# Optimization experiments

Measured on AMD Instinct MI355X. Metric: run time of the kernel, lower is better.

The kernel has to match this reference:

```python
import jax, jax.numpy as jnp
import numpy as np


def _squash(s, axis=-1, eps=1e-8):
    # squash(s) = |s|^2/(1+|s|^2) * s/|s|
    s2 = jnp.sum(s * s, axis=axis, keepdims=True)
    return (s2 / (1.0 + s2)) * s / jnp.sqrt(s2 + eps)


def _conv(x, w, b, stride):
    y = jax.lax.conv_general_dilated(
        x, w, (stride, stride), 'VALID',
        dimension_numbers=('NCHW', 'OIHW', 'NCHW'))
    return y + b[None, :, None, None]


def setup_inputs() -> dict:
    key = jax.random.key(0)
    ks = jax.random.split(key, 4)
    B = 64
    sc = 0.05
    return {
        'x': jax.random.normal(ks[0], (B, 3, 32, 32), jnp.float32),
        'conv_w': jax.random.normal(ks[1], (256, 3, 9, 9), jnp.float32) * sc,
        'conv_b': jnp.zeros((256,), jnp.float32),
        'pcap_w': jax.random.normal(ks[2], (256, 256, 9, 9), jnp.float32) * sc,
        'pcap_b': jnp.zeros((256,), jnp.float32),
        'W': jax.random.normal(ks[3], (100, 2048, 16, 8), jnp.float32) * sc,
    }


def reference(x, conv_w, conv_b, pcap_w, pcap_b, W):
    # Conv stem: [B,3,32,32] -> [B,256,24,24]
    h = jax.nn.relu(_conv(x, conv_w, conv_b, 1))
    # PrimaryCaps conv: [B,256,24,24] -> [B,256,8,8], then view to capsules
    p = _conv(h, pcap_w, pcap_b, 2)
    u = _squash(p.reshape(p.shape[0], 2048, 8))            # [B,2048,8]
    # DenseCapsule: u_hat[b,o,i,d] = W[o,i,d,k] u[b,i,k]
    u_hat = jnp.einsum('oidk,bik->boid', W, u)             # [B,100,2048,16]
    u_hat_sg = jax.lax.stop_gradient(u_hat)
    b = jnp.zeros(u_hat.shape[:3], u_hat.dtype)            # [B,100,2048]
    routings = 3
    v = None
    for i in range(routings):
        c = jax.nn.softmax(b, axis=1)                      # over out caps
        uh = u_hat if i == routings - 1 else u_hat_sg
        v = _squash(jnp.einsum('boi,boid->bod', c, uh))    # [B,100,16]
        if i < routings - 1:
            b = b + jnp.einsum('bod,boid->boi', v, u_hat_sg)
    return v
```

## Files before the change

### kernel.cpp

```cpp
#include <hip/hip_runtime.h>

#define NB 64
#define NO 100
#define NI 2048
#define ND 16
#define NK 8

#define WS_H    0
#define WS_U    9437184
#define WS_BB   10485760
#define WS_CB   23592960
#define WS_SP   36700160
#define WS_V    38338560
#define WS_PP   WS_BB

typedef __attribute__((ext_vector_type(8))) short bf16x8;
typedef __attribute__((ext_vector_type(16))) float f32x16;
typedef __attribute__((ext_vector_type(4))) float f32x4;

__device__ inline unsigned short f2bf(float x) {
    union { float f; unsigned u; } v; v.f = x;
    unsigned r = (v.u + 0x7FFFu + ((v.u >> 16) & 1u)) >> 16;
    return (unsigned short)r;
}
__device__ inline float bf2f(unsigned short h) {
    union { unsigned u; float f; } v; v.u = ((unsigned)h) << 16;
    return v.f;
}

__global__ __launch_bounds__(256) void conv1_kernel(const float* __restrict__ x,
        const float* __restrict__ w, const float* __restrict__ bias,
        unsigned short* __restrict__ h_hi, unsigned short* __restrict__ h_lo) {
    const int b = blockIdx.x;
    const int ocg = blockIdx.y;
    __shared__ float xl[3 * 32 * 32];
    __shared__ float wl[16 * 243];
    const int tid = threadIdx.x;
    for (int idx = tid; idx < 3072; idx += 256) xl[idx] = x[b * 3072 + idx];
    for (int idx = tid; idx < 16 * 243; idx += 256)
        wl[idx] = w[ocg * 16 * 243 + idx];
    __syncthreads();
    const int lane = tid & 63;
    const int wg = tid >> 6;
    float acc[4][9];
    #pragma unroll
    for (int jj = 0; jj < 4; ++jj) {
        float bv = bias[ocg * 16 + wg * 4 + jj];
        #pragma unroll
        for (int j = 0; j < 9; ++j) acc[jj][j] = bv;
    }
    int xbase[9];
    #pragma unroll
    for (int j = 0; j < 9; ++j) {
        int p = lane + 64 * j;
        xbase[j] = (p / 24) * 32 + (p % 24);
    }
    for (int ic = 0; ic < 3; ++ic)
        for (int ky = 0; ky < 9; ++ky) {
            #pragma unroll
            for (int kx = 0; kx < 9; ++kx) {
                float wv[4];
                #pragma unroll
                for (int jj = 0; jj < 4; ++jj)
                    wv[jj] = wl[(wg * 4 + jj) * 243 + ic * 81 + ky * 9 + kx];
                #pragma unroll
                for (int j = 0; j < 9; ++j) {
                    float xv = xl[ic * 1024 + xbase[j] + ky * 32 + kx];
                    #pragma unroll
                    for (int jj = 0; jj < 4; ++jj)
                        acc[jj][j] = fmaf(xv, wv[jj], acc[jj][j]);
                }
            }
        }
    #pragma unroll
    for (int jj = 0; jj < 4; ++jj) {
        int oc = ocg * 16 + wg * 4 + jj;
        #pragma unroll
        for (int j = 0; j < 9; ++j) {
            int p = lane + 64 * j;
            float v = fmaxf(acc[jj][j], 0.f);
            unsigned short hi = f2bf(v);
            unsigned short lo = f2bf(v - bf2f(hi));
            size_t o = (size_t)(b * 256 + oc) * 576 + p;
            h_hi[o] = hi;
            h_lo[o] = lo;
        }
    }
}

__global__ __launch_bounds__(256) void wb_precompute_kernel(const float* __restrict__ w,
        unsigned short* __restrict__ wBhi, unsigned short* __restrict__ wBlo) {
    const int ic = blockIdx.x;
    const int ocq = blockIdx.y;
    __shared__ float tl[64][85];
    const int tid = threadIdx.x;
    for (int f = tid; f < 5184; f += 256) {
        int oc = f / 81, kk = f % 81;
        tl[oc][kk] = w[(size_t)(ocq * 64 + oc) * 20736 + ic * 81 + kk];
    }
    __syncthreads();
    for (int idx = tid; idx < 9216; idx += 256) {
        int ky = idx >> 10;
        int rem = idx & 1023;
        int ocl = rem >> 4;
        int kx = rem & 15;
        float val = (kx < 9) ? tl[ocl][ky * 9 + kx] : 0.f;
        unsigned short hi = f2bf(val);
        unsigned short lo = f2bf(val - bf2f(hi));
        size_t dst = ((size_t)(ic * 9 + ky) * 256 + ocq * 64 + ocl) * 16 + kx;
        wBhi[dst] = hi;
        wBlo[dst] = lo;
    }
}

__global__ __launch_bounds__(256) void conv2_mfma_kernel(
        const unsigned short* __restrict__ h_hi, const unsigned short* __restrict__ h_lo,
        const unsigned short* __restrict__ wBhi, const unsigned short* __restrict__ wBlo,
        float* __restrict__ pp) {
    const int bpair = blockIdx.x;
    const int ocb = blockIdx.y;
    const int ks = blockIdx.z;
    __shared__ __align__(16) unsigned short Ahi[128 * 20];
    __shared__ __align__(16) unsigned short Alo[128 * 20];
    __shared__ __align__(16) unsigned short Bhi[128 * 20];
    __shared__ __align__(16) unsigned short Blo[128 * 20];
    const int tid = threadIdx.x;
    const int lane = tid & 63;
    const int wid = tid >> 6;
    const int wr = wid >> 1, wc = wid & 1;
    const int l31 = lane & 31, kh = lane >> 5;
    const int slot = tid & 127;
    const int role = tid >> 7;
    const int oy = (slot >> 3) & 7;
    const int ox = slot & 7;
    const unsigned short* hsel = role ? h_lo : h_hi;
    const size_t hrow0 = ((size_t)(bpair * 2 + (slot >> 6)) * 256) * 576;

    f32x16 acc[2][2];
    #pragma unroll
    for (int m = 0; m < 2; ++m)
        #pragma unroll
        for (int n = 0; n < 2; ++n)
            #pragma unroll
            for (int r = 0; r < 16; ++r) acc[m][n][r] = 0.f;

#define LDS64(arr, off, dst) { union { struct { uint2 a, b; } p; bf16x8 v; } u_;           \
    u_.p.a = *(const uint2*)((arr) + (off));                                               \
    u_.p.b = *(const uint2*)((arr) + (off) + 4);                                           \
    dst = u_.v; }

    const int ic0 = ks * 32;
    for (int ic = ic0; ic < ic0 + 32; ++ic) {
        const size_t wb_ic = (size_t)ic * 36864;
        const size_t h_ic = hrow0 + (size_t)ic * 576;
        #pragma unroll 1
        for (int ky = 0; ky < 9; ++ky) {
            __syncthreads();
            {
                const uint4* Ash = (const uint4*)(wBhi + wb_ic + (size_t)ky * 4096 + ocb * 2048);
                const uint4* Asl = (const uint4*)(wBlo + wb_ic + (size_t)ky * 4096 + ocb * 2048);
                uint4 va = Ash[tid];
                uint4 vb = Asl[tid];
                const int row = tid >> 1, half = tid & 1;
                unsigned short* dh = Ahi + row * 20 + half * 8;
                unsigned short* dl = Alo + row * 20 + half * 8;
                uint2 a0; a0.x = va.x; a0.y = va.y;
                uint2 a1; a1.x = va.z; a1.y = va.w;
                uint2 b0; b0.x = vb.x; b0.y = vb.y;
                uint2 b1; b1.x = vb.z; b1.y = vb.w;
                *(uint2*)dh = a0; *(uint2*)(dh + 4) = a1;
                *(uint2*)dl = b0; *(uint2*)(dl + 4) = b1;
            }
            {
                const unsigned int* hp =
                    (const unsigned int*)(hsel + h_ic + (2 * oy + ky) * 24 + 2 * ox);
                unsigned int d0 = hp[0], d1 = hp[1], d2 = hp[2], d3 = hp[3], d4 = hp[4];
                unsigned short* Bdst = (role ? Blo : Bhi) + slot * 20;
                uint2 p0; p0.x = d0; p0.y = d1;
                uint2 p1; p1.x = d2; p1.y = d3;
                uint2 p2; p2.x = d4 & 0xFFFFu; p2.y = 0u;
                uint2 p3; p3.x = 0u; p3.y = 0u;
                *(uint2*)Bdst = p0; *(uint2*)(Bdst + 4) = p1;
                *(uint2*)(Bdst + 8) = p2; *(uint2*)(Bdst + 12) = p3;
            }
            __syncthreads();
            bf16x8 ah[2], al[2], bh[2], bl[2];
            #pragma unroll
            for (int m = 0; m < 2; ++m) {
                const int rowoff = (wr * 64 + m * 32 + l31) * 20 + kh * 8;
                LDS64(Ahi, rowoff, ah[m]);
                LDS64(Alo, rowoff, al[m]);
            }
            #pragma unroll
            for (int n = 0; n < 2; ++n) {
                const int coloff = (wc * 64 + n * 32 + l31) * 20 + kh * 8;
                LDS64(Bhi, coloff, bh[n]);
                LDS64(Blo, coloff, bl[n]);
            }
            #pragma unroll
            for (int m = 0; m < 2; ++m)
                #pragma unroll
                for (int n = 0; n < 2; ++n) {
                    acc[m][n] = __builtin_amdgcn_mfma_f32_32x32x16_bf16(
                        ah[m], bh[n], acc[m][n], 0, 0, 0);
                    acc[m][n] = __builtin_amdgcn_mfma_f32_32x32x16_bf16(
                        ah[m], bl[n], acc[m][n], 0, 0, 0);
                    acc[m][n] = __builtin_amdgcn_mfma_f32_32x32x16_bf16(
                        al[m], bh[n], acc[m][n], 0, 0, 0);
                }
        }
    }
#undef LDS64
    #pragma unroll
    for (int m = 0; m < 2; ++m)
        #pragma unroll
        for (int n = 0; n < 2; ++n) {
            const int slotg = wc * 64 + n * 32 + l31;
            const int b = bpair * 2 + (slotg >> 6);
            const int pos = slotg & 63;
            #pragma unroll
            for (int r = 0; r < 16; ++r) {
                const int row = (r & 3) + 8 * (r >> 2) + 4 * kh;
                const int oc = ocb * 128 + wr * 64 + m * 32 + row;
                pp[(((size_t)ks * 64 + b) * 256 + oc) * 64 + pos] = acc[m][n][r];
            }
        }
}

__global__ __launch_bounds__(256) void reduce_bias_squash_kernel(
        const float* __restrict__ pp, const float* __restrict__ bias,
        float* __restrict__ u) {
    const int cap = blockIdx.x * 256 + threadIdx.x;
    const int b = cap >> 11;
    const int rem = cap & 2047;
    const int oc = rem >> 3;
    const int oy = rem & 7;
    float4 sa = {0.f, 0.f, 0.f, 0.f}, sb = {0.f, 0.f, 0.f, 0.f};
    #pragma unroll
    for (int ks = 0; ks < 8; ++ks) {
        const float4* p4 = (const float4*)&pp[(((size_t)ks * 64 + b) * 256 + oc) * 64 + oy * 8];
        float4 a = p4[0], c = p4[1];
        sa.x += a.x; sa.y += a.y; sa.z += a.z; sa.w += a.w;
        sb.x += c.x; sb.y += c.y; sb.z += c.z; sb.w += c.w;
    }
    const float bv = bias[oc];
    sa.x += bv; sa.y += bv; sa.z += bv; sa.w += bv;
    sb.x += bv; sb.y += bv; sb.z += bv; sb.w += bv;
    float s2 = sa.x * sa.x + sa.y * sa.y + sa.z * sa.z + sa.w * sa.w
             + sb.x * sb.x + sb.y * sb.y + sb.z * sb.z + sb.w * sb.w;
    float scale = (s2 / (1.f + s2)) / sqrtf(s2 + 1e-8f);
    sa.x *= scale; sa.y *= scale; sa.z *= scale; sa.w *= scale;
    sb.x *= scale; sb.y *= scale; sb.z *= scale; sb.w *= scale;
    float4* up = (float4*)&u[(size_t)cap * 8];
    up[0] = sa;
    up[1] = sb;
}

__global__ __launch_bounds__(256) void transpose_u_kernel(const float* __restrict__ u,
        float* __restrict__ ut) {
    const int blk = blockIdx.x;
    __shared__ float tl[64 * 132];
    const int tid = threadIdx.x;
    #pragma unroll
    for (int rep = 0; rep < 8; ++rep) {
        const int idx = tid + 256 * rep;
        const int b = idx >> 5, q = idx & 31;
        float4 uv = *(const float4*)(u + (size_t)b * 16384 + blk * 128 + 4 * q);
        *(float4*)&tl[b * 132 + 4 * q] = uv;
    }
    __syncthreads();
    #pragma unroll
    for (int rep = 0; rep < 32; ++rep) {
        const int row = rep * 4 + (tid >> 6);
        const int b = tid & 63;
        ut[(size_t)(blk * 128 + row) * 64 + b] = tl[b * 132 + row];
    }
}

template <int UNIFORM>
__global__ __launch_bounds__(256) void r_weighted_mfma_kernel(
        const float* __restrict__ W, const float* __restrict__ u,
        const float* __restrict__ cbuf, float* __restrict__ sp) {
    const int o = blockIdx.x;
    const int st = blockIdx.y;
    __shared__ __align__(16) unsigned short Ahi[16 * 72];
    __shared__ __align__(16) unsigned short Alo[16 * 72];
    __shared__ __align__(16) unsigned short Bhi[64 * 72];
    __shared__ __align__(16) unsigned short Blo[64 * 72];
    const int tid = threadIdx.x;
    const int lane = tid & 63;
    const int w = tid >> 6;
    const int l15 = lane & 15;
    const int hi = lane >> 4;
    const int sb = tid >> 2;
    const int si = tid & 3;
    f32x4 acc = {0.f, 0.f, 0.f, 0.f};
    const float* Wo = W + (size_t)o * 262144;
    const int i_base = st * 256;
    #pragma unroll 1
    for (int iter = 0; iter < 32; ++iter) {
        const int i0 = i_base + iter * 8;
        __syncthreads();
        {
            float4 wv = *(const float4*)(Wo + (size_t)i0 * 128 + 4 * tid);
            const int i_l = tid >> 5;
            const int d = (tid >> 1) & 15;
            const int k0 = (tid & 1) * 4;
            unsigned short* dh = Ahi + d * 72 + i_l * 8 + k0;
            unsigned short* dl = Alo + d * 72 + i_l * 8 + k0;
            float vv[4] = {wv.x, wv.y, wv.z, wv.w};
            unsigned int h01, h23, l01, l23;
            unsigned short h, l;
            h = f2bf(vv[0]); l = f2bf(vv[0] - bf2f(h)); h01 = h; l01 = l;
            h = f2bf(vv[1]); l = f2bf(vv[1] - bf2f(h)); h01 |= (unsigned)h << 16; l01 |= (unsigned)l << 16;
            h = f2bf(vv[2]); l = f2bf(vv[2] - bf2f(h)); h23 = h; l23 = l;
            h = f2bf(vv[3]); l = f2bf(vv[3] - bf2f(h)); h23 |= (unsigned)h << 16; l23 |= (unsigned)l << 16;
            *(unsigned int*)dh = h01; *(unsigned int*)(dh + 2) = h23;
            *(unsigned int*)dl = l01; *(unsigned int*)(dl + 2) = l23;
        }
        #pragma unroll
        for (int half = 0; half < 2; ++half) {
            const int i_l = si + 4 * half;
            const float* up = u + (size_t)sb * 16384 + (size_t)(i0 + i_l) * 8;
            float4 u0 = *(const float4*)up;
            float4 u1 = *(const float4*)(up + 4);
            float cv = UNIFORM ? 0.01f
                               : cbuf[(size_t)sb * (NO * NI) + o * NI + i0 + i_l];
            float q[8] = {u0.x * cv, u0.y * cv, u0.z * cv, u0.w * cv,
                          u1.x * cv, u1.y * cv, u1.z * cv, u1.w * cv};
            uint4 ph, pl;
            unsigned short h0, h1, l0, l1;
            h0 = f2bf(q[0]); l0 = f2bf(q[0] - bf2f(h0));
            h1 = f2bf(q[1]); l1 = f2bf(q[1] - bf2f(h1));
            ph.x = h0 | ((unsigned)h1 << 16); pl.x = l0 | ((unsigned)l1 << 16);
            h0 = f2bf(q[2]); l0 = f2bf(q[2] - bf2f(h0));
            h1 = f2bf(q[3]); l1 = f2bf(q[3] - bf2f(h1));
            ph.y = h0 | ((unsigned)h1 << 16); pl.y = l0 | ((unsigned)l1 << 16);
            h0 = f2bf(q[4]); l0 = f2bf(q[4] - bf2f(h0));
            h1 = f2bf(q[5]); l1 = f2bf(q[5] - bf2f(h1));
            ph.z = h0 | ((unsigned)h1 << 16); pl.z = l0 | ((unsigned)l1 << 16);
            h0 = f2bf(q[6]); l0 = f2bf(q[6] - bf2f(h0));
            h1 = f2bf(q[7]); l1 = f2bf(q[7] - bf2f(h1));
            ph.w = h0 | ((unsigned)h1 << 16); pl.w = l0 | ((unsigned)l1 << 16);
            *(uint4*)(Bhi + sb * 72 + i_l * 8) = ph;
            *(uint4*)(Blo + sb * 72 + i_l * 8) = pl;
        }
        __syncthreads();
        #pragma unroll
        for (int ch = 0; ch < 2; ++ch) {
            bf16x8 ah = *(const bf16x8*)(Ahi + l15 * 72 + ch * 32 + hi * 8);
            bf16x8 al = *(const bf16x8*)(Alo + l15 * 72 + ch * 32 + hi * 8);
            bf16x8 bh = *(const bf16x8*)(Bhi + (w * 16 + l15) * 72 + ch * 32 + hi * 8);
            bf16x8 bl = *(const bf16x8*)(Blo + (w * 16 + l15) * 72 + ch * 32 + hi * 8);
            acc = __builtin_amdgcn_mfma_f32_16x16x32_bf16(ah, bh, acc, 0, 0, 0);
            acc = __builtin_amdgcn_mfma_f32_16x16x32_bf16(ah, bl, acc, 0, 0, 0);
            acc = __builtin_amdgcn_mfma_f32_16x16x32_bf16(al, bh, acc, 0, 0, 0);
        }
    }
    const int bg = w * 16 + l15;
    float4 st4;
    st4.x = acc[0]; st4.y = acc[1]; st4.z = acc[2]; st4.w = acc[3];
    *(float4*)&sp[(((size_t)o * 8 + st) * 64 + bg) * 16 + hi * 4] = st4;
}

__global__ __launch_bounds__(256) void squash_v_kernel(const float* __restrict__ sp,
        float* __restrict__ dest) {
    const int t = blockIdx.x * 256 + threadIdx.x;
    const int d = t & 15;
    const int cap = t >> 4;
    const int o = cap >> 6;
    const int bb = cap & 63;
    float s = 0.f;
    #pragma unroll
    for (int st = 0; st < 8; ++st)
        s += sp[(((size_t)o * 8 + st) * 64 + bb) * 16 + d];
    float s2 = s * s;
    #pragma unroll
    for (int off = 1; off < 16; off <<= 1)
        s2 += __shfl_xor(s2, off, 16);
    float scale = (s2 / (1.f + s2)) / sqrtf(s2 + 1e-8f);
    dest[(bb * NO + o) * ND + d] = s * scale;
}

template <int ADD>
__global__ __launch_bounds__(256) void r_logits_mfma_kernel(
        const float* __restrict__ W, const float* __restrict__ ut,
        const float* __restrict__ v, float* __restrict__ bbuf) {
    const int o = blockIdx.x;
    const int st = blockIdx.y;
    __shared__ __align__(16) unsigned short Aext[128 * 40];
    __shared__ __align__(16) unsigned short B1[64 * 40];
    __shared__ __align__(16) unsigned short B2[64 * 40];
    __shared__ float ul[128 * 66];
    const int tid = threadIdx.x;
    const int lane = tid & 63;
    const int w = tid >> 6;
    const int l15 = lane & 15;
    const int hi = lane >> 4;
    const float* Wo = W + (size_t)o * 262144;
    {
        const int b = tid >> 2;
        const int dq = (tid & 3) * 4;
        float4 vv = *(const float4*)&v[((size_t)b * NO + o) * ND + dq];
        float q[4] = {vv.x, vv.y, vv.z, vv.w};
        #pragma unroll
        for (int c = 0; c < 4; ++c) {
            unsigned short h = f2bf(q[c]);
            unsigned short l = f2bf(q[c] - bf2f(h));
            B1[b * 40 + dq + c] = h;
            B1[b * 40 + 16 + dq + c] = h;
            B2[b * 40 + dq + c] = l;
            B2[b * 40 + 16 + dq + c] = 0;
        }
    }
    __syncthreads();
    #pragma unroll 1
    for (int iter = 0; iter < 8; ++iter) {
        __syncthreads();
        #pragma unroll
        for (int rep = 0; rep < 2; ++rep) {
            const int slot = rep * 256 + tid;
            const int i_l = slot >> 5;
            const int dgrp = (slot >> 3) & 3;
            const int k = slot & 7;
            const float* src = Wo + (size_t)(st * 128 + iter * 16 + i_l) * 128
                             + dgrp * 32 + k;
            float v0 = src[0], v1 = src[8], v2 = src[16], v3 = src[24];
            unsigned short h0 = f2bf(v0), l0 = f2bf(v0 - bf2f(h0));
            unsigned short h1 = f2bf(v1), l1 = f2bf(v1 - bf2f(h1));
            unsigned short h2 = f2bf(v2), l2 = f2bf(v2 - bf2f(h2));
            unsigned short h3 = f2bf(v3), l3 = f2bf(v3 - bf2f(h3));
            uint2 ph; ph.x = h0 | ((unsigned)h1 << 16); ph.y = h2 | ((unsigned)h3 << 16);
            uint2 pl; pl.x = l0 | ((unsigned)l1 << 16); pl.y = l2 | ((unsigned)l3 << 16);
            unsigned short* dst = Aext + (i_l * 8 + k) * 40 + dgrp * 4;
            *(uint2*)dst = ph;
            *(uint2*)(dst + 16) = pl;
        }
        const int base_row = (st * 128 + iter * 16) * 8;
        #pragma unroll
        for (int rep = 0; rep < 8; ++rep) {
            const int idx = tid + 256 * rep;
            const int row = idx >> 4, bq = idx & 15;
            float4 uv = *(const float4*)(ut + (size_t)(base_row + row) * 64 + 4 * bq);
            *(float4*)&ul[row * 66 + 4 * bq] = uv;
        }
        __syncthreads();
        f32x4 acc[8];
        bf16x8 bf1 = *(const bf16x8*)&B1[(w * 16 + l15) * 40 + hi * 8];
        bf16x8 bf2 = *(const bf16x8*)&B2[(w * 16 + l15) * 40 + hi * 8];
        #pragma unroll
        for (int mt = 0; mt < 8; ++mt) {
            f32x4 z = {0.f, 0.f, 0.f, 0.f};
            bf16x8 af = *(const bf16x8*)&Aext[(mt * 16 + l15) * 40 + hi * 8];
            z = __builtin_amdgcn_mfma_f32_16x16x32_bf16(af, bf1, z, 0, 0, 0);
            z = __builtin_amdgcn_mfma_f32_16x16x32_bf16(af, bf2, z, 0, 0, 0);
            acc[mt] = z;
        }
        #pragma unroll
        for (int mt = 0; mt < 8; ++mt) {
            float partial = 0.f;
            #pragma unroll
            for (int r = 0; r < 4; ++r) {
                const int grow = mt * 16 + hi * 4 + r;
                partial = fmaf(acc[mt][r], ul[grow * 66 + w * 16 + l15], partial);
            }
            float sum = partial + __shfl_xor(partial, 16);
            if ((hi & 1) == 0) {
                const int i_glob = st * 128 + iter * 16 + mt * 2 + (hi >> 1);
                const int bg = w * 16 + l15;
                const size_t addr = (size_t)bg * (NO * NI) + (size_t)o * NI + i_glob;
                bbuf[addr] = (ADD ? bbuf[addr] : 0.f) + sum;
            }
        }
    }
}

__global__ __launch_bounds__(256) void softmax_kernel(const float* __restrict__ bbuf,
        float* __restrict__ cbuf) {
    const int bb = blockIdx.x >> 3;
    const int i = (blockIdx.x & 7) * 256 + threadIdx.x;
    const float* col = bbuf + bb * (NO * NI) + i;
    float m = -1e30f;
    for (int o = 0; o < NO; ++o) m = fmaxf(m, col[o * NI]);
    float s = 0.f;
    for (int o = 0; o < NO; ++o) s += __expf(col[o * NI] - m);
    const float inv = 1.f / s;
    float* outp = cbuf + bb * (NO * NI) + i;
    for (int o = 0; o < NO; ++o) outp[o * NI] = __expf(col[o * NI] - m) * inv;
}

extern "C" void kernel_launch(void* const* d_in, const int* in_sizes, int n_in,
                              void* d_out, int out_size, void* d_ws, size_t ws_size,
                              hipStream_t stream) {
    (void)in_sizes; (void)n_in; (void)out_size; (void)ws_size;
    const float* x      = (const float*)d_in[0];
    const float* conv_w = (const float*)d_in[1];
    const float* conv_b = (const float*)d_in[2];
    const float* pcap_w = (const float*)d_in[3];
    const float* pcap_b = (const float*)d_in[4];
    const float* W      = (const float*)d_in[5];
    float* out = (float*)d_out;
    float* ws  = (float*)d_ws;
    unsigned short* h_hi = (unsigned short*)(ws + WS_H);
    unsigned short* h_lo = h_hi + 9437184;
    unsigned short* wBhi = (unsigned short*)(ws + WS_CB);
    unsigned short* wBlo = wBhi + 9437184;
    float* ut  = ws + WS_H;
    float* u   = ws + WS_U;
    float* bbf = ws + WS_BB;
    float* cbf = ws + WS_CB;
    float* sp  = ws + WS_SP;
    float* v   = ws + WS_V;
    float* pp  = ws + WS_PP;

    wb_precompute_kernel<<<dim3(256, 4), 256, 0, stream>>>(pcap_w, wBhi, wBlo);
    conv1_kernel<<<dim3(64, 16), 256, 0, stream>>>(x, conv_w, conv_b, h_hi, h_lo);
    conv2_mfma_kernel<<<dim3(32, 2, 8), 256, 0, stream>>>(h_hi, h_lo, wBhi, wBlo, pp);
    reduce_bias_squash_kernel<<<512, 256, 0, stream>>>(pp, pcap_b, u);
    transpose_u_kernel<<<128, 256, 0, stream>>>(u, ut);
    r_weighted_mfma_kernel<1><<<dim3(100, 8), 256, 0, stream>>>(W, u, nullptr, sp);
    squash_v_kernel<<<400, 256, 0, stream>>>(sp, v);
    r_logits_mfma_kernel<0><<<dim3(100, 16), 256, 0, stream>>>(W, ut, v, bbf);
    softmax_kernel<<<512, 256, 0, stream>>>(bbf, cbf);
    r_weighted_mfma_kernel<0><<<dim3(100, 8), 256, 0, stream>>>(W, u, cbf, sp);
    squash_v_kernel<<<400, 256, 0, stream>>>(sp, v);
    r_logits_mfma_kernel<1><<<dim3(100, 16), 256, 0, stream>>>(W, ut, v, bbf);
    softmax_kernel<<<512, 256, 0, stream>>>(bbf, cbf);
    r_weighted_mfma_kernel<0><<<dim3(100, 8), 256, 0, stream>>>(W, u, cbf, sp);
    squash_v_kernel<<<400, 256, 0, stream>>>(sp, out);
}
```

Measured before the change: 825.3 us.

## Pack conv2 K dimension as ky*10+kx per input channel, stream weights from global

```diff
diff --git a/kernel.cpp b/kernel.cpp
--- a/kernel.cpp
+++ b/kernel.cpp
@@ -89,7 +89,7 @@
 }
 
 __global__ __launch_bounds__(256) void wb_precompute_kernel(const float* __restrict__ w,
-        unsigned short* __restrict__ wBhi, unsigned short* __restrict__ wBlo) {
+        unsigned short* __restrict__ w2hi, unsigned short* __restrict__ w2lo) {
     const int ic = blockIdx.x;
     const int ocq = blockIdx.y;
     __shared__ float tl[64][85];
@@ -99,31 +99,28 @@
         tl[oc][kk] = w[(size_t)(ocq * 64 + oc) * 20736 + ic * 81 + kk];
     }
     __syncthreads();
-    for (int idx = tid; idx < 9216; idx += 256) {
-        int ky = idx >> 10;
-        int rem = idx & 1023;
-        int ocl = rem >> 4;
-        int kx = rem & 15;
-        float val = (kx < 9) ? tl[ocl][ky * 9 + kx] : 0.f;
+    for (int idx = tid; idx < 6144; idx += 256) {
+        int oc = idx / 96;
+        int kp = idx % 96;
+        int ky = kp / 10, kx = kp % 10;
+        float val = (ky < 9 && kx < 9) ? tl[oc][ky * 9 + kx] : 0.f;
         unsigned short hi = f2bf(val);
         unsigned short lo = f2bf(val - bf2f(hi));
-        size_t dst = ((size_t)(ic * 9 + ky) * 256 + ocq * 64 + ocl) * 16 + kx;
-        wBhi[dst] = hi;
-        wBlo[dst] = lo;
+        size_t dst = ((size_t)ic * 256 + ocq * 64 + oc) * 96 + kp;
+        w2hi[dst] = hi;
+        w2lo[dst] = lo;
     }
 }
 
 __global__ __launch_bounds__(256) void conv2_mfma_kernel(
         const unsigned short* __restrict__ h_hi, const unsigned short* __restrict__ h_lo,
-        const unsigned short* __restrict__ wBhi, const unsigned short* __restrict__ wBlo,
+        const unsigned short* __restrict__ w2hi, const unsigned short* __restrict__ w2lo,
         float* __restrict__ pp) {
     const int bpair = blockIdx.x;
     const int ocb = blockIdx.y;
     const int ks = blockIdx.z;
-    __shared__ __align__(16) unsigned short Ahi[128 * 20];
-    __shared__ __align__(16) unsigned short Alo[128 * 20];
-    __shared__ __align__(16) unsigned short Bhi[128 * 20];
-    __shared__ __align__(16) unsigned short Blo[128 * 20];
+    __shared__ __align__(16) unsigned short Bh[128 * 100];
+    __shared__ __align__(16) unsigned short Bl[128 * 100];
     const int tid = threadIdx.x;
     const int lane = tid & 63;
     const int wid = tid >> 6;
@@ -135,6 +132,13 @@
     const int ox = slot & 7;
     const unsigned short* hsel = role ? h_lo : h_hi;
     const size_t hrow0 = ((size_t)(bpair * 2 + (slot >> 6)) * 256) * 576;
+    const int ic0 = ks * 32;
+
+    {
+        unsigned int* Bz = (unsigned int*)((role ? Bl : Bh) + slot * 100 + 90);
+        #pragma unroll
+        for (int j = 0; j < 5; ++j) Bz[j] = 0u;
+    }
 
     f32x16 acc[2][2];
     #pragma unroll
@@ -149,65 +153,49 @@
     u_.p.b = *(const uint2*)((arr) + (off) + 4);                                           \
     dst = u_.v; }
 
-    const int ic0 = ks * 32;
-    for (int ic = ic0; ic < ic0 + 32; ++ic) {
-        const size_t wb_ic = (size_t)ic * 36864;
-        const size_t h_ic = hrow0 + (size_t)ic * 576;
-        #pragma unroll 1
-        for (int ky = 0; ky < 9; ++ky) {
-            __syncthreads();
-            {
-                const uint4* Ash = (const uint4*)(wBhi + wb_ic + (size_t)ky * 4096 + ocb * 2048);
-                const uint4* Asl = (const uint4*)(wBlo + wb_ic + (size_t)ky * 4096 + ocb * 2048);
-                uint4 va = Ash[tid];
-                uint4 vb = Asl[tid];
-                const int row = tid >> 1, half = tid & 1;
-                unsigned short* dh = Ahi + row * 20 + half * 8;
-                unsigned short* dl = Alo + row * 20 + half * 8;
-                uint2 a0; a0.x = va.x; a0.y = va.y;
-                uint2 a1; a1.x = va.z; a1.y = va.w;
-                uint2 b0; b0.x = vb.x; b0.y = vb.y;
-                uint2 b1; b1.x = vb.z; b1.y = vb.w;
-                *(uint2*)dh = a0; *(uint2*)(dh + 4) = a1;
-                *(uint2*)dl = b0; *(uint2*)(dl + 4) = b1;
-            }
-            {
+    #pragma unroll 1
+    for (int ic_l = 0; ic_l < 32; ++ic_l) {
+        const int ic = ic0 + ic_l;
+        __syncthreads();
+        {
+            const size_t h_ic = hrow0 + (size_t)ic * 576;
+            unsigned int* Brow = (unsigned int*)((role ? Bl : Bh) + slot * 100);
+            #pragma unroll
+            for (int ky = 0; ky < 9; ++ky) {
                 const unsigned int* hp =
                     (const unsigned int*)(hsel + h_ic + (2 * oy + ky) * 24 + 2 * ox);
-                unsigned int d0 = hp[0], d1 = hp[1], d2 = hp[2], d3 = hp[3], d4 = hp[4];
-                unsigned short* Bdst = (role ? Blo : Bhi) + slot * 20;
-                uint2 p0; p0.x = d0; p0.y = d1;
-                uint2 p1; p1.x = d2; p1.y = d3;
-                uint2 p2; p2.x = d4 & 0xFFFFu; p2.y = 0u;
-                uint2 p3; p3.x = 0u; p3.y = 0u;
-                *(uint2*)Bdst = p0; *(uint2*)(Bdst + 4) = p1;
-                *(uint2*)(Bdst + 8) = p2; *(uint2*)(Bdst + 12) = p3;
+                unsigned int* dst = Brow + 5 * ky;
+                dst[0] = hp[0]; dst[1] = hp[1]; dst[2] = hp[2];
+                dst[3] = hp[3]; dst[4] = hp[4];
             }
-            __syncthreads();
-            bf16x8 ah[2], al[2], bh[2], bl[2];
-            #pragma unroll
-            for (int m = 0; m < 2; ++m) {
-                const int rowoff = (wr * 64 + m * 32 + l31) * 20 + kh * 8;
-                LDS64(Ahi, rowoff, ah[m]);
-                LDS64(Alo, rowoff, al[m]);
-            }
-            #pragma unroll
-            for (int n = 0; n < 2; ++n) {
-                const int coloff = (wc * 64 + n * 32 + l31) * 20 + kh * 8;
-                LDS64(Bhi, coloff, bh[n]);
-                LDS64(Blo, coloff, bl[n]);
-            }
-            #pragma unroll
-            for (int m = 0; m < 2; ++m)
-                #pragma unroll
-                for (int n = 0; n < 2; ++n) {
-                    acc[m][n] = __builtin_amdgcn_mfma_f32_32x32x16_bf16(
-                        ah[m], bh[n], acc[m][n], 0, 0, 0);
-                    acc[m][n] = __builtin_amdgcn_mfma_f32_32x32x16_bf16(
-                        ah[m], bl[n], acc[m][n], 0, 0, 0);
-                    acc[m][n] = __builtin_amdgcn_mfma_f32_32x32x16_bf16(
-                        al[m], bh[n], acc[m][n], 0, 0, 0);
-                }
+        }
+        __syncthreads();
+        const size_t wbase = ((size_t)ic * 256 + ocb * 128) * 96;
+        #pragma unroll
+        for (int c = 0; c < 6; ++c) {
+            const size_t a0 = wbase + (size_t)(wr * 64 + l31) * 96 + 16 * c + 8 * kh;
+            const size_t a1 = a0 + 32 * 96;
+            bf16x8 ah0 = *(const bf16x8*)(w2hi + a0);
+            bf16x8 ah1 = *(const bf16x8*)(w2hi + a1);
+            bf16x8 al0 = *(const bf16x8*)(w2lo + a0);
+            bf16x8 al1 = *(const bf16x8*)(w2lo + a1);
+            bf16x8 bh0, bh1, bl0, bl1;
+            const int b0 = (wc * 64 + l31) * 100 + 16 * c + 8 * kh;
+            const int b1 = b0 + 32 * 100;
+            LDS64(Bh, b0, bh0); LDS64(Bh, b1, bh1);
+            LDS64(Bl, b0, bl0); LDS64(Bl, b1, bl1);
+            acc[0][0] = __builtin_amdgcn_mfma_f32_32x32x16_bf16(ah0, bh0, acc[0][0], 0, 0, 0);
+            acc[0][0] = __builtin_amdgcn_mfma_f32_32x32x16_bf16(ah0, bl0, acc[0][0], 0, 0, 0);
+            acc[0][0] = __builtin_amdgcn_mfma_f32_32x32x16_bf16(al0, bh0, acc[0][0], 0, 0, 0);
+            acc[0][1] = __builtin_amdgcn_mfma_f32_32x32x16_bf16(ah0, bh1, acc[0][1], 0, 0, 0);
+            acc[0][1] = __builtin_amdgcn_mfma_f32_32x32x16_bf16(ah0, bl1, acc[0][1], 0, 0, 0);
+            acc[0][1] = __builtin_amdgcn_mfma_f32_32x32x16_bf16(al0, bh1, acc[0][1], 0, 0, 0);
+            acc[1][0] = __builtin_amdgcn_mfma_f32_32x32x16_bf16(ah1, bh0, acc[1][0], 0, 0, 0);
+            acc[1][0] = __builtin_amdgcn_mfma_f32_32x32x16_bf16(ah1, bl0, acc[1][0], 0, 0, 0);
+            acc[1][0] = __builtin_amdgcn_mfma_f32_32x32x16_bf16(al1, bh0, acc[1][0], 0, 0, 0);
+            acc[1][1] = __builtin_amdgcn_mfma_f32_32x32x16_bf16(ah1, bh1, acc[1][1], 0, 0, 0);
+            acc[1][1] = __builtin_amdgcn_mfma_f32_32x32x16_bf16(ah1, bl1, acc[1][1], 0, 0, 0);
+            acc[1][1] = __builtin_amdgcn_mfma_f32_32x32x16_bf16(al1, bh1, acc[1][1], 0, 0, 0);
         }
     }
 #undef LDS64
@@ -503,8 +491,8 @@
     float* ws  = (float*)d_ws;
     unsigned short* h_hi = (unsigned short*)(ws + WS_H);
     unsigned short* h_lo = h_hi + 9437184;
-    unsigned short* wBhi = (unsigned short*)(ws + WS_CB);
-    unsigned short* wBlo = wBhi + 9437184;
+    unsigned short* w2hi = (unsigned short*)(ws + WS_CB);
+    unsigned short* w2lo = w2hi + 6291456;
     float* ut  = ws + WS_H;
     float* u   = ws + WS_U;
     float* bbf = ws + WS_BB;
@@ -513,9 +501,9 @@
     float* v   = ws + WS_V;
     float* pp  = ws + WS_PP;
 
-    wb_precompute_kernel<<<dim3(256, 4), 256, 0, stream>>>(pcap_w, wBhi, wBlo);
+    wb_precompute_kernel<<<dim3(256, 4), 256, 0, stream>>>(pcap_w, w2hi, w2lo);
     conv1_kernel<<<dim3(64, 16), 256, 0, stream>>>(x, conv_w, conv_b, h_hi, h_lo);
-    conv2_mfma_kernel<<<dim3(32, 2, 8), 256, 0, stream>>>(h_hi, h_lo, wBhi, wBlo, pp);
+    conv2_mfma_kernel<<<dim3(32, 2, 8), 256, 0, stream>>>(h_hi, h_lo, w2hi, w2lo, pp);
     reduce_bias_squash_kernel<<<512, 256, 0, stream>>>(pp, pcap_b, u);
     transpose_u_kernel<<<128, 256, 0, stream>>>(u, ut);
     r_weighted_mfma_kernel<1><<<dim3(100, 8), 256, 0, stream>>>(W, u, nullptr, sp);
```

After: 780.0 us. -5.5%, faster.
